# Kernel optimization log

Measured on AMD Instinct MI355X. Metric: run time of the kernel, lower is better.

The kernel has to match this reference:

```python
import jax, jax.numpy as jnp
import numpy as np

N = 50000      # nodes
E = 1600000    # directed edges (avg degree 32)
IN_DIM = 64
OUT_DIM = 64


def setup_inputs() -> dict:
    key = jax.random.key(0)
    ks = jax.random.split(key, 8)
    mu = jax.random.normal(ks[0], (N, IN_DIM), dtype=jnp.float32)
    x = jax.random.normal(ks[1], (N, 1), dtype=jnp.float32)
    edge_index = jax.random.randint(ks[2], (2, E), 0, N, dtype=jnp.int64)
    edge_w = jax.random.uniform(ks[3], (E,), dtype=jnp.float32)
    # torch nn.Linear(in, out, bias=False) weight has shape [out, in]
    W1 = jax.random.normal(ks[4], (OUT_DIM, 1), dtype=jnp.float32) * (1.0 / 1.0)
    W2 = jax.random.normal(ks[5], (OUT_DIM, 1), dtype=jnp.float32) * (1.0 / 1.0)
    W3 = jax.random.normal(ks[6], (OUT_DIM, IN_DIM), dtype=jnp.float32) * (1.0 / np.sqrt(IN_DIM))
    W4 = jax.random.normal(ks[7], (OUT_DIM, 3 * OUT_DIM), dtype=jnp.float32) * (1.0 / np.sqrt(3 * OUT_DIM))
    return {"mu": mu, "x": x, "edge_index": edge_index, "edge_w": edge_w,
            "W1": W1, "W2": W2, "W3": W3, "W4": W4}


def reference(mu, x, edge_index, edge_w, W1, W2, W3, W4):
    relu = jax.nn.relu
    n_nodes = mu.shape[0]
    # per-node / per-edge embeddings
    h_x = relu(x @ W1.T)                       # [N, out]
    h_e = relu(edge_w[:, None] @ W2.T)         # [E, out]
    h_mu = relu(mu @ W3.T)                     # [N, out]
    dst = edge_index[1]                        # gather side (reverse-direction message passing)
    src = edge_index[0]                        # scatter side
    # gather, concat along feature dim -> [E, 3*out]
    cat_feat = jnp.concatenate([h_x[dst], h_e, h_mu[dst]], axis=1)
    # scatter_add over destination row 0 -> [N, 3*out]
    agg = jax.ops.segment_sum(cat_feat, src, num_segments=n_nodes)
    agg = relu(agg @ W4.T)                     # [N, out]
    return relu(h_x + h_mu + agg)
```

## Files before the change

kernel.cpp:

```cpp
#include <hip/hip_runtime.h>


#define KBINS 512
#define BCHUNK 4096
#define CAPB 4096
#define CAPL 3500
#define MAXW 98

typedef __attribute__((ext_vector_type(8))) short short8;
typedef __attribute__((ext_vector_type(4))) float f32x4;

__device__ inline unsigned short to_bf16(float f) {
    unsigned u = __float_as_uint(f);
    return (unsigned short)((u + 0x7FFFu + ((u >> 16) & 1u)) >> 16);
}

__global__ void k_prep(const float* __restrict__ W1, const float* __restrict__ W2,
                       const float* __restrict__ W3, const float* __restrict__ W4,
                       short* __restrict__ gB1, short* __restrict__ gB2,
                       float* __restrict__ gvec, unsigned* __restrict__ gcursor) {
    __shared__ float sa[64], sb[64];
    int t = threadIdx.x;
    gcursor[t] = 0u;
    gcursor[256 + t] = 0u;
    if (t < 64) {
        float w1 = W1[t];
        sa[t] = fmaxf(w1, 0.f);
        sb[t] = fmaxf(-w1, 0.f);
        gvec[t] = sa[t];
        gvec[64 + t] = sb[t];
    }
    __syncthreads();
    if (t < 64) {
        float s1 = 0.f, s2 = 0.f, s3 = 0.f;
#pragma unroll 8
        for (int o = 0; o < 64; ++o) {
            float w4a = W4[t * 192 + o];
            float w4b = W4[t * 192 + 64 + o];
            s1 += w4a * sa[o];
            s2 += w4a * sb[o];
            s3 += w4b * fmaxf(W2[o], 0.f);
        }
        gvec[128 + t] = s1;
        gvec[192 + t] = s2;
        gvec[256 + t] = s3;
    }
    for (int idx = t; idx < 4096; idx += 256) {
        int j = idx >> 6, k = idx & 63;
        int lane = ((k >> 3) & 3) * 16 + (j & 15);
        int pos = (((j >> 4) * 2 + (k >> 5)) * 64 + lane) * 8 + (k & 7);
        gB1[pos] = (short)to_bf16(W3[idx]);
        gB2[pos] = (short)to_bf16(W4[j * 192 + 128 + k]);
    }
}

__global__ void __launch_bounds__(512, 8) k_hb(
    const float* __restrict__ mu, const float* __restrict__ x,
    const short* __restrict__ gB1, const short* __restrict__ gB2,
    const float* __restrict__ gvec,
    unsigned short* __restrict__ base, unsigned short* __restrict__ hc2,
    const int* __restrict__ ei, const float* __restrict__ ew,
    unsigned* __restrict__ gcursor, unsigned* __restrict__ bins,
    int N, int E) {
    __shared__ __align__(16) char smem[35840];
    short* sB1 = (short*)smem;
    short* sB2 = (short*)(smem + 8192);
    float* sAv = (float*)(smem + 16384);
    float* sBv = (float*)(smem + 16640);
    float* sVA = (float*)(smem + 16896);
    float* sVB = (float*)(smem + 17152);
    short* sA  = (short*)(smem + 17408);
    unsigned* cnt   = (unsigned*)smem;
    unsigned* basel = (unsigned*)(smem + 2048);
    unsigned* gbase = (unsigned*)(smem + 4096);
    unsigned* wsum  = (unsigned*)(smem + 6144);
    unsigned* wpre  = (unsigned*)(smem + 6176);
    unsigned* stage = (unsigned*)(smem + 6208);
    unsigned short* binof = (unsigned short*)(smem + 22592);

    int t = threadIdx.x;
    int wave = t >> 6, l = t & 63;

    for (int i = t; i < 512; i += 512) {
        ((short8*)sB1)[i] = ((const short8*)gB1)[i];
        ((short8*)sB2)[i] = ((const short8*)gB2)[i];
    }
    if (t >= 512 - 256) {
        int v = t - (512 - 256);
        if (v < 64) sAv[v] = gvec[v];
        else if (v < 128) sBv[v - 64] = gvec[64 + (v - 64)];
        else if (v < 192) sVA[v - 128] = gvec[128 + (v - 128)];
        else sVB[v - 192] = gvec[192 + (v - 192)];
    }
    __syncthreads();

    int n0 = (blockIdx.x * 8 + wave) * 16;
    if (n0 < N) {
        short* A1 = sA + wave * 2304 / 2;
        {
            int srow = l >> 2, scol = (l & 3) * 16;
            bool rok = (n0 + srow) < N;
            const float4* gp = (const float4*)(mu + (size_t)(n0 + srow) * 64 + scol);
            float4 m0 = {}, m1 = {}, m2 = {}, m3 = {};
            if (rok) { m0 = gp[0]; m1 = gp[1]; m2 = gp[2]; m3 = gp[3]; }
            short8 v0, v1;
            v0[0]=to_bf16(m0.x); v0[1]=to_bf16(m0.y); v0[2]=to_bf16(m0.z); v0[3]=to_bf16(m0.w);
            v0[4]=to_bf16(m1.x); v0[5]=to_bf16(m1.y); v0[6]=to_bf16(m1.z); v0[7]=to_bf16(m1.w);
            v1[0]=to_bf16(m2.x); v1[1]=to_bf16(m2.y); v1[2]=to_bf16(m2.z); v1[3]=to_bf16(m2.w);
            v1[4]=to_bf16(m3.x); v1[5]=to_bf16(m3.y); v1[6]=to_bf16(m3.z); v1[7]=to_bf16(m3.w);
            *(short8*)&A1[srow * 72 + scol] = v0;
            *(short8*)&A1[srow * 72 + scol + 8] = v1;
        }
        float pr[4], qr[4];
#pragma unroll
        for (int r = 0; r < 4; ++r) {
            int nr = n0 + (l >> 4) * 4 + r;
            float xv = (nr < N) ? x[nr] : 0.f;
            pr[r] = fmaxf(xv, 0.f);
            qr[r] = fmaxf(-xv, 0.f);
        }
        f32x4 acc[4] = {};
        {
            short8 a0 = *(const short8*)&A1[(l & 15) * 72 + ((l >> 4) * 8)];
            short8 a1 = *(const short8*)&A1[(l & 15) * 72 + 32 + ((l >> 4) * 8)];
#pragma unroll
            for (int jt = 0; jt < 4; ++jt) {
                short8 b0 = *(const short8*)&sB1[((jt * 2 + 0) * 64 + l) * 8];
                short8 b1 = *(const short8*)&sB1[((jt * 2 + 1) * 64 + l) * 8];
                acc[jt] = __builtin_amdgcn_mfma_f32_16x16x32_bf16(a0, b0, acc[jt], 0, 0, 0);
                acc[jt] = __builtin_amdgcn_mfma_f32_16x16x32_bf16(a1, b1, acc[jt], 0, 0, 0);
            }
        }
#pragma unroll
        for (int jt = 0; jt < 4; ++jt) {
            int jc = jt * 16 + (l & 15);
            float aj = sAv[jc], bj = sBv[jc];
#pragma unroll
            for (int r = 0; r < 4; ++r) {
                int row = (l >> 4) * 4 + r;
                float h = fmaxf(acc[jt][r], 0.f);
                A1[row * 72 + jc] = (short)to_bf16(h);
                int nr = n0 + row;
                if (nr < N) base[(size_t)nr * 64 + jc] = to_bf16(pr[r] * aj + qr[r] * bj + h);
            }
        }
        f32x4 acc2[4] = {};
        {
            short8 a0 = *(const short8*)&A1[(l & 15) * 72 + ((l >> 4) * 8)];
            short8 a1 = *(const short8*)&A1[(l & 15) * 72 + 32 + ((l >> 4) * 8)];
#pragma unroll
            for (int jt = 0; jt < 4; ++jt) {
                short8 b0 = *(const short8*)&sB2[((jt * 2 + 0) * 64 + l) * 8];
                short8 b1 = *(const short8*)&sB2[((jt * 2 + 1) * 64 + l) * 8];
                acc2[jt] = __builtin_amdgcn_mfma_f32_16x16x32_bf16(a0, b0, acc2[jt], 0, 0, 0);
                acc2[jt] = __builtin_amdgcn_mfma_f32_16x16x32_bf16(a1, b1, acc2[jt], 0, 0, 0);
            }
        }
#pragma unroll
        for (int jt = 0; jt < 4; ++jt) {
            int jc = jt * 16 + (l & 15);
            float vaj = sVA[jc], vbj = sVB[jc];
#pragma unroll
            for (int r = 0; r < 4; ++r) {
                int nr = n0 + (l >> 4) * 4 + r;
                if (nr < N)
                    hc2[(size_t)nr * 64 + jc] =
                        to_bf16(acc2[jt][r] + pr[r] * vaj + qr[r] * vbj);
            }
        }
    }
    __syncthreads();

    for (int c0 = blockIdx.x * BCHUNK; c0 < E; c0 += gridDim.x * BCHUNK) {
        cnt[t] = 0;
        __syncthreads();
        int mybin[8]; unsigned myrank[8]; unsigned myrec[8]; bool ok[8];
#pragma unroll
        for (int k = 0; k < 8; ++k) {
            int e = c0 + t + k * 512;
            ok[k] = (e < E);
            if (ok[k]) {
                int s = ei[e];
                int d = ei[E + e];
                unsigned wq = (unsigned)(ew[e] * 512.0f + 0.5f);
                if (wq > 511u) wq = 511u;
                unsigned b = ((unsigned)s * (unsigned)KBINS) / (unsigned)N;
                unsigned start = ((unsigned)b * (unsigned)N + KBINS - 1) / KBINS;
                unsigned sl = (unsigned)s - start;
                myrec[k] = (unsigned)d | (sl << 16) | (wq << 23);
                mybin[k] = (int)b;
                myrank[k] = atomicAdd(&cnt[b], 1u);
            }
        }
        __syncthreads();
        {
            unsigned v = cnt[t];
            unsigned sc = v;
#pragma unroll
            for (int off = 1; off < 64; off <<= 1) {
                unsigned u = (unsigned)__shfl_up((int)sc, off, 64);
                if (l >= off) sc += u;
            }
            if (l == 63) wsum[wave] = sc;
            __syncthreads();
            if (t < 8) {
                unsigned s = 0;
                for (int i = 0; i < t; ++i) s += wsum[i];
                wpre[t] = s;
            }
            __syncthreads();
            unsigned excl = sc - v + wpre[wave];
            basel[t] = excl;
            if (v) gbase[t] = atomicAdd(&gcursor[t], v);
        }
        __syncthreads();
#pragma unroll
        for (int k = 0; k < 8; ++k) if (ok[k]) {
            unsigned pos = basel[mybin[k]] + myrank[k];
            stage[pos] = myrec[k];
            binof[pos] = (unsigned short)mybin[k];
        }
        __syncthreads();
        int total = E - c0; if (total > BCHUNK) total = BCHUNK;
#pragma unroll
        for (int k = 0; k < 8; ++k) {
            int i = t + k * 512;
            if (i < total) {
                int b = binof[i];
                unsigned dst = gbase[b] + (unsigned)i - basel[b];
                if (dst < CAPB) bins[(size_t)b * CAPB + dst] = stage[i];
            }
        }
        __syncthreads();
    }
}

__global__ void __launch_bounds__(1024) k_agg(
    const unsigned short* __restrict__ hc2, const unsigned short* __restrict__ base,
    const unsigned* __restrict__ gcursor, const unsigned* __restrict__ bins,
    const float* __restrict__ gvec, float* __restrict__ out, int N) {
    __shared__ unsigned srec[CAPL];
    __shared__ unsigned hist[128];
    __shared__ unsigned sbase[128];
    __shared__ float svs[64];
    int b = blockIdx.x;
    int t = threadIdx.x;
    if (t < 128) hist[t] = 0;
    if (t >= 128 && t < 192) svs[t - 128] = gvec[256 + (t - 128)];
    int start = (b * N + KBINS - 1) / KBINS;
    int endn  = ((b + 1) * N + KBINS - 1) / KBINS;
    if (endn > N) endn = N;
    int W = endn - start;
    if (W > MAXW) W = MAXW;
    __syncthreads();
    int cntb = (int)gcursor[b];
    if (cntb > CAPB) cntb = CAPB;
    const unsigned* rec = bins + (size_t)b * CAPB;
    unsigned r[4]; unsigned rank[4]; bool ok[4];
#pragma unroll
    for (int k = 0; k < 4; ++k) {
        int i = t + k * 1024;
        ok[k] = (i < cntb);
        if (ok[k]) {
            r[k] = rec[i];
            rank[k] = atomicAdd(&hist[(r[k] >> 16) & 0x7Fu], 1u);
        }
    }
    __syncthreads();
    if (t < 128) sbase[t] = hist[t];
    __syncthreads();
    for (int off = 1; off < 128; off <<= 1) {
        unsigned u = 0;
        if (t < 128 && t >= off) u = sbase[t - off];
        __syncthreads();
        if (t < 128) sbase[t] += u;
        __syncthreads();
    }
    if (t < 128) sbase[t] -= hist[t];
    __syncthreads();
#pragma unroll
    for (int k = 0; k < 4; ++k) if (ok[k]) {
        unsigned pos = sbase[(r[k] >> 16) & 0x7Fu] + rank[k];
        if (pos < CAPL) srec[pos] = r[k];
    }
    __syncthreads();
    int wave = t >> 6, j = t & 63;
    float vsj = svs[j] * (1.0f / 512.0f);
    for (int sl = wave; sl < W; sl += 16) {
        int beg = (int)sbase[sl];
        int end = beg + (int)hist[sl];
        if (beg > CAPL) beg = CAPL;
        if (end > CAPL) end = CAPL;
        float acc = 0.f, swn = 0.f;
        int i = beg;
        for (; i + 8 <= end; i += 8) {
            unsigned r0 = srec[i + 0], r1 = srec[i + 1], r2 = srec[i + 2], r3 = srec[i + 3];
            unsigned r4 = srec[i + 4], r5 = srec[i + 5], r6 = srec[i + 6], r7 = srec[i + 7];
            unsigned u0 = hc2[(size_t)(r0 & 0xFFFFu) * 64 + j];
            unsigned u1 = hc2[(size_t)(r1 & 0xFFFFu) * 64 + j];
            unsigned u2 = hc2[(size_t)(r2 & 0xFFFFu) * 64 + j];
            unsigned u3 = hc2[(size_t)(r3 & 0xFFFFu) * 64 + j];
            unsigned u4 = hc2[(size_t)(r4 & 0xFFFFu) * 64 + j];
            unsigned u5 = hc2[(size_t)(r5 & 0xFFFFu) * 64 + j];
            unsigned u6 = hc2[(size_t)(r6 & 0xFFFFu) * 64 + j];
            unsigned u7 = hc2[(size_t)(r7 & 0xFFFFu) * 64 + j];
            acc += __uint_as_float(u0 << 16) + __uint_as_float(u1 << 16)
                 + __uint_as_float(u2 << 16) + __uint_as_float(u3 << 16)
                 + __uint_as_float(u4 << 16) + __uint_as_float(u5 << 16)
                 + __uint_as_float(u6 << 16) + __uint_as_float(u7 << 16);
            swn += (float)(r0 >> 23) + (float)(r1 >> 23)
                 + (float)(r2 >> 23) + (float)(r3 >> 23)
                 + (float)(r4 >> 23) + (float)(r5 >> 23)
                 + (float)(r6 >> 23) + (float)(r7 >> 23);
        }
        for (; i < end; ++i) {
            unsigned rr = srec[i];
            acc += __uint_as_float(((unsigned)hc2[(size_t)(rr & 0xFFFFu) * 64 + j]) << 16);
            swn += (float)(rr >> 23);
        }
        float agg = fmaxf(swn * vsj + acc, 0.f);
        size_t gi = (size_t)(start + sl) * 64 + j;
        float bval = __uint_as_float(((unsigned)base[gi]) << 16);
        out[gi] = fmaxf(bval + agg, 0.f);
    }
}

extern "C" void kernel_launch(void* const* d_in, const int* in_sizes, int n_in,
                              void* d_out, int out_size, void* d_ws, size_t ws_size,
                              hipStream_t stream) {
    const float* mu = (const float*)d_in[0];
    const float* x  = (const float*)d_in[1];
    const int*   ei = (const int*)d_in[2];
    const float* ew = (const float*)d_in[3];
    const float* W1 = (const float*)d_in[4];
    const float* W2 = (const float*)d_in[5];
    const float* W3 = (const float*)d_in[6];
    const float* W4 = (const float*)d_in[7];
    float* out = (float*)d_out;

    const int N = in_sizes[1];
    const int E = in_sizes[3];

    unsigned short* base = (unsigned short*)d_ws;
    unsigned short* hc2 = base + (size_t)N * 64;
    unsigned* bins = (unsigned*)(hc2 + (size_t)N * 64);
    unsigned* gcursor = bins + (size_t)KBINS * CAPB;
    short* gB1 = (short*)(gcursor + KBINS);
    short* gB2 = gB1 + 4096;
    float* gvec = (float*)(gB2 + 4096);

    k_prep<<<1, 256, 0, stream>>>(W1, W2, W3, W4, gB1, gB2, gvec, gcursor);

    int hblocks = (N + 127) / 128;
    int chunks = (E + BCHUNK - 1) / BCHUNK;
    int grid = hblocks > chunks ? hblocks : chunks;
    k_hb<<<grid, 512, 0, stream>>>(mu, x, gB1, gB2, gvec, base, hc2,
                                   ei, ew, gcursor, bins, N, E);

    k_agg<<<KBINS, 1024, 0, stream>>>(hc2, base, gcursor, bins, gvec, out, N);
}
```

Baseline: 68.32 us.

## Vectorize aggregation gathers to 8-byte loads across lane groups and shuffle-scan histogram

The aggregation loop now splits each wave into four 16-lane groups. Each lane loads four bf16 features with one 8-byte load, and each group handles a different edge, with partial sums combined by xor shuffles at the end. This cuts per-lane gather instruction count and exposes more independent memory requests per edge. The 128-bin exclusive prefix scan is replaced with a single-wave shuffle scan, which removes many block-wide barriers. The cost is extra shuffle reductions and only a quarter of the lanes doing the output store.

New measurement: 59.76 us. 12.5% less time.

```diff
diff --git a/kernel.cpp b/kernel.cpp
--- a/kernel.cpp
+++ b/kernel.cpp
@@ -9,6 +9,7 @@
 
 typedef __attribute__((ext_vector_type(8))) short short8;
 typedef __attribute__((ext_vector_type(4))) float f32x4;
+typedef __attribute__((ext_vector_type(4))) unsigned short u16x4;
 
 __device__ inline unsigned short to_bf16(float f) {
     unsigned u = __float_as_uint(f);
@@ -242,7 +243,7 @@
     __shared__ unsigned srec[CAPL];
     __shared__ unsigned hist[128];
     __shared__ unsigned sbase[128];
-    __shared__ float svs[64];
+    __shared__ __align__(16) float svs[64];
     int b = blockIdx.x;
     int t = threadIdx.x;
     if (t < 128) hist[t] = 0;
@@ -267,16 +268,17 @@
         }
     }
     __syncthreads();
-    if (t < 128) sbase[t] = hist[t];
-    __syncthreads();
-    for (int off = 1; off < 128; off <<= 1) {
-        unsigned u = 0;
-        if (t < 128 && t >= off) u = sbase[t - off];
-        __syncthreads();
-        if (t < 128) sbase[t] += u;
-        __syncthreads();
-    }
-    if (t < 128) sbase[t] -= hist[t];
+    if (t < 64) {
+        unsigned h0 = hist[2 * t], h1 = hist[2 * t + 1];
+        unsigned s = h0 + h1;
+#pragma unroll
+        for (int off = 1; off < 64; off <<= 1) {
+            unsigned u = (unsigned)__shfl_up((int)s, off, 64);
+            if (t >= off) s += u;
+        }
+        sbase[2 * t]     = s - h1 - h0;
+        sbase[2 * t + 1] = s - h1;
+    }
     __syncthreads();
 #pragma unroll
     for (int k = 0; k < 4; ++k) if (ok[k]) {
@@ -284,44 +286,64 @@
         if (pos < CAPL) srec[pos] = r[k];
     }
     __syncthreads();
-    int wave = t >> 6, j = t & 63;
-    float vsj = svs[j] * (1.0f / 512.0f);
+    int wave = t >> 6, l = t & 63;
+    int g = l >> 4, m = l & 15;
+    f32x4 vsv = *(const f32x4*)&svs[m * 4];
+    const float sc512 = 1.0f / 512.0f;
     for (int sl = wave; sl < W; sl += 16) {
         int beg = (int)sbase[sl];
         int end = beg + (int)hist[sl];
         if (beg > CAPL) beg = CAPL;
         if (end > CAPL) end = CAPL;
-        float acc = 0.f, swn = 0.f;
+        f32x4 acc = {0.f, 0.f, 0.f, 0.f};
+        float swn = 0.f;
         int i = beg;
         for (; i + 8 <= end; i += 8) {
-            unsigned r0 = srec[i + 0], r1 = srec[i + 1], r2 = srec[i + 2], r3 = srec[i + 3];
-            unsigned r4 = srec[i + 4], r5 = srec[i + 5], r6 = srec[i + 6], r7 = srec[i + 7];
-            unsigned u0 = hc2[(size_t)(r0 & 0xFFFFu) * 64 + j];
-            unsigned u1 = hc2[(size_t)(r1 & 0xFFFFu) * 64 + j];
-            unsigned u2 = hc2[(size_t)(r2 & 0xFFFFu) * 64 + j];
-            unsigned u3 = hc2[(size_t)(r3 & 0xFFFFu) * 64 + j];
-            unsigned u4 = hc2[(size_t)(r4 & 0xFFFFu) * 64 + j];
-            unsigned u5 = hc2[(size_t)(r5 & 0xFFFFu) * 64 + j];
-            unsigned u6 = hc2[(size_t)(r6 & 0xFFFFu) * 64 + j];
-            unsigned u7 = hc2[(size_t)(r7 & 0xFFFFu) * 64 + j];
-            acc += __uint_as_float(u0 << 16) + __uint_as_float(u1 << 16)
-                 + __uint_as_float(u2 << 16) + __uint_as_float(u3 << 16)
-                 + __uint_as_float(u4 << 16) + __uint_as_float(u5 << 16)
-                 + __uint_as_float(u6 << 16) + __uint_as_float(u7 << 16);
-            swn += (float)(r0 >> 23) + (float)(r1 >> 23)
-                 + (float)(r2 >> 23) + (float)(r3 >> 23)
-                 + (float)(r4 >> 23) + (float)(r5 >> 23)
-                 + (float)(r6 >> 23) + (float)(r7 >> 23);
-        }
-        for (; i < end; ++i) {
-            unsigned rr = srec[i];
-            acc += __uint_as_float(((unsigned)hc2[(size_t)(rr & 0xFFFFu) * 64 + j]) << 16);
-            swn += (float)(rr >> 23);
-        }
-        float agg = fmaxf(swn * vsj + acc, 0.f);
-        size_t gi = (size_t)(start + sl) * 64 + j;
-        float bval = __uint_as_float(((unsigned)base[gi]) << 16);
-        out[gi] = fmaxf(bval + agg, 0.f);
+            unsigned r0 = srec[i + g];
+            unsigned r1 = srec[i + 4 + g];
+            u16x4 u0 = *(const u16x4*)(hc2 + (size_t)(r0 & 0xFFFFu) * 64 + m * 4);
+            u16x4 u1 = *(const u16x4*)(hc2 + (size_t)(r1 & 0xFFFFu) * 64 + m * 4);
+            acc[0] += __uint_as_float((unsigned)u0[0] << 16);
+            acc[1] += __uint_as_float((unsigned)u0[1] << 16);
+            acc[2] += __uint_as_float((unsigned)u0[2] << 16);
+            acc[3] += __uint_as_float((unsigned)u0[3] << 16);
+            acc[0] += __uint_as_float((unsigned)u1[0] << 16);
+            acc[1] += __uint_as_float((unsigned)u1[1] << 16);
+            acc[2] += __uint_as_float((unsigned)u1[2] << 16);
+            acc[3] += __uint_as_float((unsigned)u1[3] << 16);
+            swn += (float)(r0 >> 23) + (float)(r1 >> 23);
+        }
+        for (; i < end; i += 4) {
+            if (i + g < end) {
+                unsigned r0 = srec[i + g];
+                u16x4 u0 = *(const u16x4*)(hc2 + (size_t)(r0 & 0xFFFFu) * 64 + m * 4);
+                acc[0] += __uint_as_float((unsigned)u0[0] << 16);
+                acc[1] += __uint_as_float((unsigned)u0[1] << 16);
+                acc[2] += __uint_as_float((unsigned)u0[2] << 16);
+                acc[3] += __uint_as_float((unsigned)u0[3] << 16);
+                swn += (float)(r0 >> 23);
+            }
+        }
+#pragma unroll
+        for (int off = 16; off < 64; off <<= 1) {
+            acc[0] += __shfl_xor(acc[0], off, 64);
+            acc[1] += __shfl_xor(acc[1], off, 64);
+            acc[2] += __shfl_xor(acc[2], off, 64);
+            acc[3] += __shfl_xor(acc[3], off, 64);
+            swn    += __shfl_xor(swn, off, 64);
+        }
+        if (g == 0) {
+            size_t gi = (size_t)(start + sl) * 64 + m * 4;
+            u16x4 bv = *(const u16x4*)(base + gi);
+            f32x4 o;
+#pragma unroll
+            for (int k = 0; k < 4; ++k) {
+                float aggv = fmaxf(swn * (vsv[k] * sc512) + acc[k], 0.f);
+                float bval = __uint_as_float(((unsigned)bv[k]) << 16);
+                o[k] = fmaxf(bval + aggv, 0.f);
+            }
+            *(f32x4*)&out[gi] = o;
+        }
     }
 }
 
```
